# Kernel tuning notes

Hardware: AMD Instinct MI355X
Metric: run time of the kernel (lower is better)

Reference implementation:

```python
import jax, jax.numpy as jnp
import numpy as np

B, N, K, D = 4096, 64, 48, 64   # batch, n_features, n_bins, d_embedding
F = N * D                        # flattened embedding dim
E, H, O = 8, 1024, 512           # experts, expert hidden, expert out
T, TH = 2, 256                   # tasks, tower hidden


def setup_inputs() -> dict:
    key = jax.random.key(0)
    ks = jax.random.split(key, 10)
    # PLE buffers from uniform bins linspace(0,1,K+1): w = 1/width, b = -edge/width
    edges = jnp.linspace(0.0, 1.0, K + 1)
    width = jnp.diff(edges)
    w = 1.0 / width                      # (K,)
    b = -edges[:-1] / width              # (K,)
    ple_weight = jnp.broadcast_to(w, (N, K)).astype(jnp.float32)
    ple_bias = jnp.broadcast_to(b, (N, K)).astype(jnp.float32)
    s = lambda fan_in: fan_in ** -0.5
    return {
        "x": jax.random.uniform(ks[0], (B, N), jnp.float32),
        "ple_weight": ple_weight,
        "ple_bias": ple_bias,
        "emb_W": jax.random.normal(ks[1], (N, K, D), jnp.float32) * s(K),
        "emb_b": jax.random.normal(ks[2], (N, D), jnp.float32) * s(K),
        "gate_W": jax.random.normal(ks[3], (F, E), jnp.float32) * s(F),
        "gate_b": jnp.zeros((E,), jnp.float32),
        "e_W1": jax.random.normal(ks[4], (E, F, H), jnp.float32) * s(F),
        "e_b1": jnp.zeros((E, H), jnp.float32),
        "e_W2": jax.random.normal(ks[5], (E, H, O), jnp.float32) * s(H),
        "e_b2": jnp.zeros((E, O), jnp.float32),
        "tw1": jax.random.normal(ks[6], (T, O, TH), jnp.float32) * s(O),
        "tb1": jnp.zeros((T, TH), jnp.float32),
        "tw2": jax.random.normal(ks[7], (T, TH, 1), jnp.float32) * s(TH),
        "tb2": jnp.zeros((T, 1), jnp.float32),
        "top_k": 2,
    }


def reference(x, ple_weight, ple_bias, emb_W, emb_b, gate_W, gate_b,
              e_W1, e_b1, e_W2, e_b2, tw1, tb1, tw2, tb2, top_k):
    # --- Piecewise Linear Encoding: (B, N) -> (B, N, K) ---
    enc = ple_bias + ple_weight * x[..., None]
    enc = jnp.concatenate([
        jnp.minimum(enc[..., :1], 1.0),
        jnp.clip(enc[..., 1:-1], 0.0, 1.0),
        jnp.maximum(enc[..., -1:], 0.0),
    ], axis=-1)
    # --- PLE embeddings via NLinear + ReLU: (B, N, K) -> (B, N, D) ---
    emb = jax.nn.relu(jnp.einsum("bnk,nkd->bnd", enc, emb_W) + emb_b)
    flat = emb.reshape(emb.shape[0], -1)                 # (B, F)
    # --- Sparse MoE gating (softmax + top-k renormalized) ---
    probs = jax.nn.softmax(flat @ gate_W + gate_b, axis=-1)   # (B, E)
    topv, topi = jax.lax.top_k(probs, top_k)
    topv = topv / jnp.sum(topv, axis=-1, keepdims=True)
    gates = jnp.zeros_like(probs).at[jnp.arange(probs.shape[0])[:, None], topi].set(topv)
    # --- Experts (computed densely, gated combine) ---
    h = jax.nn.relu(jnp.einsum("bf,efh->beh", flat, e_W1) + e_b1)   # (B, E, H)
    eo = jnp.einsum("beh,eho->beo", h, e_W2) + e_b2                 # (B, E, O)
    moe = jnp.einsum("be,beo->bo", gates, eo)                       # (B, O)
    # --- Task towers: per-task MLP -> scalar ---
    th = jax.nn.relu(jnp.einsum("bo,tos->bts", moe, tw1) + tb1)     # (B, T, TH)
    out = (jnp.einsum("bts,tsu->btu", th, tw2) + tb2)[..., 0]       # (B, T)
    return out
```

## Files before the change

### kernel.cpp

```cpp
#include <hip/hip_runtime.h>
#include <cstdint>

#define B_ 4096
#define N_ 64
#define K_ 48
#define D_ 64
#define F_ 4096
#define E_ 8
#define H_ 1024
#define O_ 512
#define T_ 2
#define TH_ 256
#define NSLOT (B_ * 2)

#define MAXT1 72
#define MAXT2 136

typedef float f32x4 __attribute__((ext_vector_type(4)));
typedef __bf16 bf16x8 __attribute__((ext_vector_type(8)));

__device__ __forceinline__ unsigned short f2bf(float f) {
    union { float f; unsigned int u; } v; v.f = f;
    unsigned int u = v.u;
    u += 0x7FFFu + ((u >> 16) & 1u);
    return (unsigned short)(u >> 16);
}

__device__ __forceinline__ void gload_lds16(const void* gptr, void* lptr) {
    auto* g = reinterpret_cast<const __attribute__((address_space(1))) unsigned int*>(
        reinterpret_cast<uintptr_t>(gptr));
    auto* l = reinterpret_cast<__attribute__((address_space(3))) unsigned int*>(
        reinterpret_cast<uintptr_t>(lptr));
    __builtin_amdgcn_global_load_lds(g, l, 16, 0, 0);
}

__global__ __launch_bounds__(64) void prefix_kernel(
    const float* __restrict__ embW, const float* __restrict__ embB,
    float* __restrict__ P)
{
    int n = blockIdx.x;
    int lane = threadIdx.x;
    float acc = embB[n * D_ + lane];
    const float* wsrc = embW + (size_t)n * K_ * D_ + lane;
    float* dst = P + (size_t)n * K_ * D_ + lane;
    #pragma unroll 8
    for (int k = 0; k < K_; ++k) {
        dst[k * D_] = acc;
        acc += wsrc[k * D_];
    }
}

__global__ __launch_bounds__(256) void ple_embed_kernel(
    const float* __restrict__ x, const float* __restrict__ plw,
    const float* __restrict__ plb, const float* __restrict__ embW,
    const float* __restrict__ P, const float* __restrict__ gateW,
    unsigned short* __restrict__ flat_bf, float* __restrict__ logits)
{
    __shared__ float gpart[4][E_];
    int b = blockIdx.x;
    int tid = threadIdx.x, lane = tid & 63, w = tid >> 6;

    float xl = x[b * N_ + lane];
    float gp[E_];
    #pragma unroll
    for (int e = 0; e < E_; ++e) gp[e] = 0.0f;

    #pragma unroll 4
    for (int i = 0; i < 16; ++i) {
        int n = w * 16 + i;
        float xn = __shfl(xl, n);
        const float* pw = plw + n * K_;
        const float* pb = plb + n * K_;
        float t = fmaf(pw[0], xn, pb[0]);
        int j = (int)t;
        j = max(0, min(K_ - 1, j));
        float f = fminf(fmaxf(fmaf(pw[j], xn, pb[j]), 0.0f), 1.0f);
        size_t base = ((size_t)n * K_ + j) * D_ + lane;
        float emb = fmaxf(fmaf(f, embW[base], P[base]), 0.0f);
        flat_bf[(size_t)b * F_ + n * D_ + lane] = f2bf(emb);

        const float4* gw4 = (const float4*)(gateW + (size_t)(n * D_ + lane) * E_);
        float4 g0 = gw4[0], g1 = gw4[1];
        gp[0] = fmaf(emb, g0.x, gp[0]);
        gp[1] = fmaf(emb, g0.y, gp[1]);
        gp[2] = fmaf(emb, g0.z, gp[2]);
        gp[3] = fmaf(emb, g0.w, gp[3]);
        gp[4] = fmaf(emb, g1.x, gp[4]);
        gp[5] = fmaf(emb, g1.y, gp[5]);
        gp[6] = fmaf(emb, g1.z, gp[6]);
        gp[7] = fmaf(emb, g1.w, gp[7]);
    }

    #pragma unroll
    for (int off = 32; off > 0; off >>= 1) {
        #pragma unroll
        for (int e = 0; e < E_; ++e) gp[e] += __shfl_down(gp[e], off);
    }
    if (lane == 0) {
        #pragma unroll
        for (int e = 0; e < E_; ++e) gpart[w][e] = gp[e];
    }
    __syncthreads();
    if (tid < E_)
        logits[b * E_ + tid] =
            gpart[0][tid] + gpart[1][tid] + gpart[2][tid] + gpart[3][tid];
}

__global__ __launch_bounds__(256) void gate_top2_kernel(
    const float* __restrict__ logits, const float* __restrict__ gate_b,
    int* __restrict__ topi, float* __restrict__ topg, int* __restrict__ counts)
{
    int b = blockIdx.x * 256 + threadIdx.x;
    int lane = threadIdx.x & 63;
    float l[E_];
    #pragma unroll
    for (int e = 0; e < E_; ++e) l[e] = logits[b * E_ + e] + gate_b[e];
    int e1 = 0; float v1 = l[0];
    #pragma unroll
    for (int e = 1; e < E_; ++e) if (l[e] > v1) { v1 = l[e]; e1 = e; }
    int e2 = -1; float v2 = -1e30f;
    #pragma unroll
    for (int e = 0; e < E_; ++e) if (e != e1 && l[e] > v2) { v2 = l[e]; e2 = e; }
    float ex = expf(v2 - v1);
    float g1 = 1.0f / (1.0f + ex);
    float g2 = ex / (1.0f + ex);
    topi[b * 2] = e1; topi[b * 2 + 1] = e2;
    topg[b * 2] = g1; topg[b * 2 + 1] = g2;
    #pragma unroll
    for (int e = 0; e < E_; ++e) {
        unsigned long long m1 = __ballot(e1 == e);
        unsigned long long m2 = __ballot(e2 == e);
        if (lane == 0) {
            int c = __popcll(m1) + __popcll(m2);
            if (c) atomicAdd(&counts[e], c);
        }
    }
}

__global__ void scan_kernel(const int* __restrict__ counts, int* __restrict__ offsets,
                            int* __restrict__ tiles1, int* __restrict__ tiles2,
                            int* __restrict__ ntiles) {
    if (threadIdx.x == 0) {
        int s = 0, n1 = 0, n2 = 0;
        for (int e = 0; e < E_; ++e) {
            offsets[e] = s;
            int c = counts[e];
            for (int tr = 0; tr * 128 < c; ++tr) tiles1[n1++] = (e << 16) | tr;
            for (int tr = 0; tr * 64 < c; ++tr) tiles2[n2++] = (e << 16) | tr;
            s += c;
        }
        offsets[E_] = s;
        ntiles[0] = n1;
        ntiles[1] = n2;
    }
}

__global__ __launch_bounds__(256) void scatter_kernel(
    const int* __restrict__ topi, const float* __restrict__ topg,
    const int* __restrict__ offsets, int* __restrict__ cursors,
    int* __restrict__ rows, float* __restrict__ gatev)
{
    int b = blockIdx.x * 256 + threadIdx.x;
    int lane = threadIdx.x & 63;
    #pragma unroll
    for (int j = 0; j < 2; ++j) {
        int e = topi[b * 2 + j];
        float g = topg[b * 2 + j];
        #pragma unroll
        for (int ex = 0; ex < E_; ++ex) {
            unsigned long long m = __ballot(e == ex);
            if (e == ex) {
                int leader = __builtin_ctzll(m);
                int base = 0;
                if (lane == leader) base = atomicAdd(&cursors[ex], __popcll(m));
                base = __shfl(base, leader);
                int pos = base + __popcll(m & ((1ull << lane) - 1ull));
                int slot = offsets[ex] + pos;
                rows[slot] = b;
                gatev[slot] = g;
            }
        }
    }
}

__global__ __launch_bounds__(256) void transp_bf16_kernel(
    const float* __restrict__ in, unsigned short* __restrict__ out, int R, int C)
{
    __shared__ float tile[64][65];
    int ch = blockIdx.z;
    const float* src = in + (size_t)ch * R * C;
    unsigned short* dst = out + (size_t)ch * R * C;
    int c0 = blockIdx.x * 64, r0 = blockIdx.y * 64;
    int lane = threadIdx.x & 63, w = threadIdx.x >> 6;
    #pragma unroll
    for (int i = 0; i < 16; ++i) {
        int r = w * 16 + i;
        tile[r][lane] = src[(size_t)(r0 + r) * C + c0 + lane];
    }
    __syncthreads();
    #pragma unroll
    for (int i = 0; i < 16; ++i) {
        int c = w * 16 + i;
        dst[(size_t)(c0 + c) * R + r0 + lane] = f2bf(tile[lane][c]);
    }
}

__global__ __launch_bounds__(256) void fc1_kernel(
    const unsigned short* __restrict__ Abf,
    const unsigned short* __restrict__ Wbt,
    const float* __restrict__ bias,
    const int* __restrict__ rows, const int* __restrict__ offsets,
    const int* __restrict__ tiles1, const int* __restrict__ ntiles,
    unsigned short* __restrict__ Hbf)
{
    int bid = blockIdx.x;
    int tile = bid >> 4, cn = bid & 15;
    if (tile >= ntiles[0]) return;
    int te = tiles1[tile];
    int e = te >> 16, tr = te & 0xffff;
    int m0 = offsets[e], mEnd = offsets[e + 1];
    int Me = mEnd - m0;

    __shared__ alignas(16) unsigned short As[128 * 64];
    __shared__ alignas(16) unsigned short Bs[64 * 64];

    int tid = threadIdx.x, lane = tid & 63, wv = tid >> 6;
    int lr = lane >> 3;
    int pchunk = lane & 7;
    int cg = pchunk ^ lr;

    const unsigned short* aptr[4];
    const unsigned short* bptr[2];
    #pragma unroll
    for (int i = 0; i < 4; ++i) {
        int rowA = (wv * 4 + i) * 8 + lr;
        int slot = min(m0 + tr * 128 + rowA, mEnd - 1);
        aptr[i] = Abf + (size_t)rows[slot] * F_ + cg * 8;
    }
    #pragma unroll
    for (int i = 0; i < 2; ++i) {
        int rowB = cn * 64 + (wv * 2 + i) * 8 + lr;
        bptr[i] = Wbt + ((size_t)e * H_ + rowB) * (size_t)F_ + cg * 8;
    }

    f32x4 zero = {0.f, 0.f, 0.f, 0.f};
    f32x4 acc[4][2];
    #pragma unroll
    for (int i = 0; i < 4; ++i)
        #pragma unroll
        for (int j = 0; j < 2; ++j) acc[i][j] = zero;

    int wvM = wv >> 1, wvN = wv & 1;
    int m16 = lane & 15, q = lane >> 4;

    for (int k0 = 0; k0 < F_; k0 += 64) {
        __syncthreads();
        #pragma unroll
        for (int i = 0; i < 4; ++i)
            gload_lds16(aptr[i] + k0, &As[(wv * 4 + i) * 512]);
        #pragma unroll
        for (int i = 0; i < 2; ++i)
            gload_lds16(bptr[i] + k0, &Bs[(wv * 2 + i) * 512]);
        __syncthreads();
        #pragma unroll
        for (int ks = 0; ks < 2; ++ks) {
            bf16x8 af[4], bfg[2];
            #pragma unroll
            for (int mt = 0; mt < 4; ++mt) {
                int m = wvM * 64 + mt * 16 + m16;
                int pos = (ks * 4 + q) ^ (m & 7);
                af[mt] = *(const bf16x8*)&As[m * 64 + pos * 8];
            }
            #pragma unroll
            for (int nt = 0; nt < 2; ++nt) {
                int n = wvN * 32 + nt * 16 + m16;
                int pos = (ks * 4 + q) ^ (n & 7);
                bfg[nt] = *(const bf16x8*)&Bs[n * 64 + pos * 8];
            }
            #pragma unroll
            for (int mt = 0; mt < 4; ++mt)
                #pragma unroll
                for (int nt = 0; nt < 2; ++nt)
                    acc[mt][nt] = __builtin_amdgcn_mfma_f32_16x16x32_bf16(
                        af[mt], bfg[nt], acc[mt][nt], 0, 0, 0);
        }
    }

    #pragma unroll
    for (int nt = 0; nt < 2; ++nt) {
        int col = cn * 64 + wvN * 32 + nt * 16 + m16;
        float bv = bias[e * H_ + col];
        #pragma unroll
        for (int mt = 0; mt < 4; ++mt) {
            int rbase = tr * 128 + wvM * 64 + mt * 16 + q * 4;
            #pragma unroll
            for (int r = 0; r < 4; ++r) {
                int rr = rbase + r;
                if (rr < Me) {
                    float v = fmaxf(acc[mt][nt][r] + bv, 0.0f);
                    Hbf[(size_t)(m0 + rr) * H_ + col] = f2bf(v);
                }
            }
        }
    }
}

__global__ __launch_bounds__(256) void fc2_kernel(
    const unsigned short* __restrict__ Hbf,
    const unsigned short* __restrict__ Wbt,
    const float* __restrict__ bias,
    const int* __restrict__ rows, const float* __restrict__ gatev,
    const int* __restrict__ offsets, const int* __restrict__ tiles2,
    const int* __restrict__ ntiles, float* __restrict__ moe)
{
    int bid = blockIdx.x;
    int tile = bid >> 3, cn = bid & 7;
    if (tile >= ntiles[1]) return;
    int te = tiles2[tile];
    int e = te >> 16, tr = te & 0xffff;
    int m0 = offsets[e], mEnd = offsets[e + 1];
    int Me = mEnd - m0;

    __shared__ alignas(16) unsigned short As[64 * 64];
    __shared__ alignas(16) unsigned short Bs[64 * 64];

    int tid = threadIdx.x, lane = tid & 63, wv = tid >> 6;
    int lr = lane >> 3;
    int pchunk = lane & 7;
    int cg = pchunk ^ lr;

    const unsigned short* aptr[2];
    const unsigned short* bptr[2];
    #pragma unroll
    for (int i = 0; i < 2; ++i) {
        int rowA = (wv * 2 + i) * 8 + lr;
        int slot = min(m0 + tr * 64 + rowA, mEnd - 1);
        aptr[i] = Hbf + (size_t)slot * H_ + cg * 8;
        int rowB = cn * 64 + (wv * 2 + i) * 8 + lr;
        bptr[i] = Wbt + ((size_t)e * O_ + rowB) * (size_t)H_ + cg * 8;
    }

    f32x4 zero = {0.f, 0.f, 0.f, 0.f};
    f32x4 acc[4];
    #pragma unroll
    for (int i = 0; i < 4; ++i) acc[i] = zero;

    int m16 = lane & 15, q = lane >> 4;

    for (int k0 = 0; k0 < H_; k0 += 64) {
        __syncthreads();
        #pragma unroll
        for (int i = 0; i < 2; ++i) {
            gload_lds16(aptr[i] + k0, &As[(wv * 2 + i) * 512]);
            gload_lds16(bptr[i] + k0, &Bs[(wv * 2 + i) * 512]);
        }
        __syncthreads();
        #pragma unroll
        for (int ks = 0; ks < 2; ++ks) {
            bf16x8 af[4], bfg;
            #pragma unroll
            for (int mt = 0; mt < 4; ++mt) {
                int m = mt * 16 + m16;
                int pos = (ks * 4 + q) ^ (m & 7);
                af[mt] = *(const bf16x8*)&As[m * 64 + pos * 8];
            }
            {
                int n = wv * 16 + m16;
                int pos = (ks * 4 + q) ^ (n & 7);
                bfg = *(const bf16x8*)&Bs[n * 64 + pos * 8];
            }
            #pragma unroll
            for (int mt = 0; mt < 4; ++mt)
                acc[mt] = __builtin_amdgcn_mfma_f32_16x16x32_bf16(
                    af[mt], bfg, acc[mt], 0, 0, 0);
        }
    }

    int col = cn * 64 + wv * 16 + m16;
    float bv = bias[e * O_ + col];
    #pragma unroll
    for (int mt = 0; mt < 4; ++mt) {
        int rbase = tr * 64 + mt * 16 + q * 4;
        #pragma unroll
        for (int r = 0; r < 4; ++r) {
            int rr = rbase + r;
            if (rr < Me) {
                int slot = m0 + rr;
                float g = gatev[slot];
                int b = rows[slot];
                atomicAdd(&moe[(size_t)b * O_ + col], g * (acc[mt][r] + bv));
            }
        }
    }
}

__global__ __launch_bounds__(256) void tower1_kernel(
    const float* __restrict__ moe, const float* __restrict__ tw1,
    const float* __restrict__ tb1, float* __restrict__ th)
{
    __shared__ float ms[16 * O_];
    int b0 = blockIdx.x * 16;
    int tid = threadIdx.x;
    for (int idx = tid; idx < 16 * O_; idx += 256)
        ms[idx] = moe[(size_t)b0 * O_ + idx];
    __syncthreads();

    int s = tid;
    float acc0[16], acc1[16];
    float bv0 = tb1[s], bv1 = tb1[TH_ + s];
    #pragma unroll
    for (int i = 0; i < 16; ++i) { acc0[i] = bv0; acc1[i] = bv1; }

    for (int o = 0; o < O_; o += 4) {
        float w0[4], w1[4];
        #pragma unroll
        for (int u = 0; u < 4; ++u) {
            w0[u] = tw1[(size_t)(o + u) * TH_ + s];
            w1[u] = tw1[(size_t)(O_ + o + u) * TH_ + s];
        }
        #pragma unroll
        for (int smp = 0; smp < 16; ++smp) {
            float4 mv = *(const float4*)&ms[smp * O_ + o];
            acc0[smp] = fmaf(mv.x, w0[0], acc0[smp]);
            acc0[smp] = fmaf(mv.y, w0[1], acc0[smp]);
            acc0[smp] = fmaf(mv.z, w0[2], acc0[smp]);
            acc0[smp] = fmaf(mv.w, w0[3], acc0[smp]);
            acc1[smp] = fmaf(mv.x, w1[0], acc1[smp]);
            acc1[smp] = fmaf(mv.y, w1[1], acc1[smp]);
            acc1[smp] = fmaf(mv.z, w1[2], acc1[smp]);
            acc1[smp] = fmaf(mv.w, w1[3], acc1[smp]);
        }
    }
    #pragma unroll
    for (int smp = 0; smp < 16; ++smp) {
        int b = b0 + smp;
        th[((size_t)b * T_ + 0) * TH_ + s] = fmaxf(acc0[smp], 0.0f);
        th[((size_t)b * T_ + 1) * TH_ + s] = fmaxf(acc1[smp], 0.0f);
    }
}

__global__ __launch_bounds__(256) void tower2_kernel(
    const float* __restrict__ th, const float* __restrict__ tw2,
    const float* __restrict__ tb2, float* __restrict__ out)
{
    int tid = threadIdx.x, lane = tid & 63, w = tid >> 6;
    int pair = blockIdx.x * 4 + w;
    int t = pair & 1;
    const float* tp = th + (size_t)pair * TH_;
    float p = 0.0f;
    #pragma unroll
    for (int j = 0; j < TH_ / 64; ++j) {
        int s = lane + j * 64;
        p = fmaf(tp[s], tw2[t * TH_ + s], p);
    }
    #pragma unroll
    for (int off = 32; off > 0; off >>= 1) p += __shfl_down(p, off);
    if (lane == 0) out[pair] = p + tb2[t];
}

extern "C" void kernel_launch(void* const* d_in, const int* in_sizes, int n_in,
                              void* d_out, int out_size, void* d_ws, size_t ws_size,
                              hipStream_t stream)
{
    const float* x     = (const float*)d_in[0];
    const float* plw   = (const float*)d_in[1];
    const float* plb   = (const float*)d_in[2];
    const float* embW  = (const float*)d_in[3];
    const float* embB  = (const float*)d_in[4];
    const float* gateW = (const float*)d_in[5];
    const float* gateB = (const float*)d_in[6];
    const float* eW1   = (const float*)d_in[7];
    const float* eB1   = (const float*)d_in[8];
    const float* eW2   = (const float*)d_in[9];
    const float* eB2   = (const float*)d_in[10];
    const float* tw1   = (const float*)d_in[11];
    const float* tb1   = (const float*)d_in[12];
    const float* tw2   = (const float*)d_in[13];
    const float* tb2   = (const float*)d_in[14];
    float* out = (float*)d_out;

    char* w = (char*)d_ws;
    auto alloc = [&](size_t bytes) {
        char* p = w; w += (bytes + 255) & ~(size_t)255; return p;
    };
    unsigned short* flat_bf = (unsigned short*)alloc((size_t)B_ * F_ * 2);
    unsigned short* W1bt    = (unsigned short*)alloc((size_t)E_ * H_ * F_ * 2);
    unsigned short* W2bt    = (unsigned short*)alloc((size_t)E_ * O_ * H_ * 2);
    unsigned short* Hbf     = (unsigned short*)alloc((size_t)NSLOT * H_ * 2);
    float* Ppre    = (float*)alloc((size_t)N_ * K_ * D_ * 4);
    float* logits  = (float*)alloc((size_t)B_ * E_ * 4);
    float* moe     = (float*)alloc((size_t)B_ * O_ * 4);
    float* th      = (float*)alloc((size_t)B_ * T_ * TH_ * 4);
    int*   topi    = (int*)alloc((size_t)B_ * 2 * 4);
    float* topg    = (float*)alloc((size_t)B_ * 2 * 4);
    int*   rows    = (int*)alloc((size_t)NSLOT * 4);
    float* gatev   = (float*)alloc((size_t)NSLOT * 4);
    int*   counts  = (int*)alloc(E_ * 4);
    int*   offsets = (int*)alloc((E_ + 1) * 4);
    int*   cursors = (int*)alloc(E_ * 4);
    int*   tiles1  = (int*)alloc(MAXT1 * 4);
    int*   tiles2  = (int*)alloc(MAXT2 * 4);
    int*   ntiles  = (int*)alloc(2 * 4);

    hipMemsetAsync(moe, 0, (size_t)B_ * O_ * 4, stream);
    hipMemsetAsync(counts, 0, E_ * 4, stream);
    hipMemsetAsync(cursors, 0, E_ * 4, stream);

    prefix_kernel<<<N_, 64, 0, stream>>>(embW, embB, Ppre);
    ple_embed_kernel<<<B_, 256, 0, stream>>>(x, plw, plb, embW, Ppre, gateW,
                                             flat_bf, logits);
    transp_bf16_kernel<<<dim3(H_ / 64, F_ / 64, E_), 256, 0, stream>>>(eW1, W1bt, F_, H_);
    transp_bf16_kernel<<<dim3(O_ / 64, H_ / 64, E_), 256, 0, stream>>>(eW2, W2bt, H_, O_);
    gate_top2_kernel<<<B_ / 256, 256, 0, stream>>>(logits, gateB, topi, topg, counts);
    scan_kernel<<<1, 64, 0, stream>>>(counts, offsets, tiles1, tiles2, ntiles);
    scatter_kernel<<<B_ / 256, 256, 0, stream>>>(topi, topg, offsets, cursors, rows, gatev);
    fc1_kernel<<<MAXT1 * 16, 256, 0, stream>>>(flat_bf, W1bt, eB1, rows, offsets,
                                               tiles1, ntiles, Hbf);
    fc2_kernel<<<MAXT2 * 8, 256, 0, stream>>>(Hbf, W2bt, eB2, rows, gatev, offsets,
                                              tiles2, ntiles, moe);
    tower1_kernel<<<B_ / 16, 256, 0, stream>>>(moe, tw1, tb1, th);
    tower2_kernel<<<B_ * T_ / 4, 256, 0, stream>>>(th, tw2, tb2, out);
}
```

Baseline: 601.1 us.

## Enlarge expert GEMM tiles, parallelize scan, and fuse tower kernels

The fc1 tile grows from 128x64 to 128x128 output per block, with 4x4 MFMA accumulators per wave, so each weight tile is reused across more rows and fewer blocks are launched. fc2 now uses 128-row tiles that share the fc1 tile list, which removes the second tile list. The scan kernel computes offsets and tile entries with one thread per expert instead of a serial loop. The two tower kernels become one kernel that reduces the second layer in-block, removing the th intermediate buffer. In exchange, fc1 uses more registers and shared memory and launches fewer blocks, and the fused tower kernel runs at 8 rows per block.

```diff
diff --git a/kernel.cpp b/kernel.cpp
--- a/kernel.cpp
+++ b/kernel.cpp
@@ -14,7 +14,6 @@
 #define NSLOT (B_ * 2)
 
 #define MAXT1 72
-#define MAXT2 136
 
 typedef float f32x4 __attribute__((ext_vector_type(4)));
 typedef __bf16 bf16x8 __attribute__((ext_vector_type(8)));
@@ -138,21 +137,23 @@
 }
 
 __global__ void scan_kernel(const int* __restrict__ counts, int* __restrict__ offsets,
-                            int* __restrict__ tiles1, int* __restrict__ tiles2,
-                            int* __restrict__ ntiles) {
-    if (threadIdx.x == 0) {
-        int s = 0, n1 = 0, n2 = 0;
-        for (int e = 0; e < E_; ++e) {
-            offsets[e] = s;
-            int c = counts[e];
-            for (int tr = 0; tr * 128 < c; ++tr) tiles1[n1++] = (e << 16) | tr;
-            for (int tr = 0; tr * 64 < c; ++tr) tiles2[n2++] = (e << 16) | tr;
-            s += c;
-        }
-        offsets[E_] = s;
-        ntiles[0] = n1;
-        ntiles[1] = n2;
-    }
+                            int* __restrict__ tiles1, int* __restrict__ ntiles) {
+    int e = threadIdx.x;
+    if (e >= E_) return;
+    int c[E_];
+    #pragma unroll
+    for (int i = 0; i < E_; ++i) c[i] = counts[i];
+    int off = 0, tb = 0, tot = 0, ttot = 0;
+    #pragma unroll
+    for (int i = 0; i < E_; ++i) {
+        int t = (c[i] + 127) >> 7;
+        if (i < e) { off += c[i]; tb += t; }
+        tot += c[i]; ttot += t;
+    }
+    offsets[e] = off;
+    if (e == 0) { offsets[E_] = tot; ntiles[0] = ttot; }
+    int nt = (c[e] + 127) >> 7;
+    for (int tr = 0; tr < nt; ++tr) tiles1[tb + tr] = (e << 16) | tr;
 }
 
 __global__ __launch_bounds__(256) void scatter_kernel(
@@ -214,7 +215,7 @@
     unsigned short* __restrict__ Hbf)
 {
     int bid = blockIdx.x;
-    int tile = bid >> 4, cn = bid & 15;
+    int tile = bid >> 3, cn = bid & 7;
     if (tile >= ntiles[0]) return;
     int te = tiles1[tile];
     int e = te >> 16, tr = te & 0xffff;
@@ -222,7 +223,7 @@
     int Me = mEnd - m0;
 
     __shared__ alignas(16) unsigned short As[128 * 64];
-    __shared__ alignas(16) unsigned short Bs[64 * 64];
+    __shared__ alignas(16) unsigned short Bs[128 * 64];
 
     int tid = threadIdx.x, lane = tid & 63, wv = tid >> 6;
     int lr = lane >> 3;
@@ -230,25 +231,23 @@
     int cg = pchunk ^ lr;
 
     const unsigned short* aptr[4];
-    const unsigned short* bptr[2];
+    const unsigned short* bptr[4];
     #pragma unroll
     for (int i = 0; i < 4; ++i) {
-        int rowA = (wv * 4 + i) * 8 + lr;
+        int reg = wv * 4 + i;
+        int rowA = reg * 8 + lr;
         int slot = min(m0 + tr * 128 + rowA, mEnd - 1);
         aptr[i] = Abf + (size_t)rows[slot] * F_ + cg * 8;
-    }
-    #pragma unroll
-    for (int i = 0; i < 2; ++i) {
-        int rowB = cn * 64 + (wv * 2 + i) * 8 + lr;
+        int rowB = cn * 128 + reg * 8 + lr;
         bptr[i] = Wbt + ((size_t)e * H_ + rowB) * (size_t)F_ + cg * 8;
     }
 
     f32x4 zero = {0.f, 0.f, 0.f, 0.f};
-    f32x4 acc[4][2];
+    f32x4 acc[4][4];
     #pragma unroll
     for (int i = 0; i < 4; ++i)
         #pragma unroll
-        for (int j = 0; j < 2; ++j) acc[i][j] = zero;
+        for (int j = 0; j < 4; ++j) acc[i][j] = zero;
 
     int wvM = wv >> 1, wvN = wv & 1;
     int m16 = lane & 15, q = lane >> 4;
@@ -256,15 +255,15 @@
     for (int k0 = 0; k0 < F_; k0 += 64) {
         __syncthreads();
         #pragma unroll
-        for (int i = 0; i < 4; ++i)
-            gload_lds16(aptr[i] + k0, &As[(wv * 4 + i) * 512]);
-        #pragma unroll
-        for (int i = 0; i < 2; ++i)
-            gload_lds16(bptr[i] + k0, &Bs[(wv * 2 + i) * 512]);
+        for (int i = 0; i < 4; ++i) {
+            int reg = wv * 4 + i;
+            gload_lds16(aptr[i] + k0, &As[reg * 512]);
+            gload_lds16(bptr[i] + k0, &Bs[reg * 512]);
+        }
         __syncthreads();
         #pragma unroll
         for (int ks = 0; ks < 2; ++ks) {
-            bf16x8 af[4], bfg[2];
+            bf16x8 af[4], bfg[4];
             #pragma unroll
             for (int mt = 0; mt < 4; ++mt) {
                 int m = wvM * 64 + mt * 16 + m16;
@@ -272,23 +271,23 @@
                 af[mt] = *(const bf16x8*)&As[m * 64 + pos * 8];
             }
             #pragma unroll
-            for (int nt = 0; nt < 2; ++nt) {
-                int n = wvN * 32 + nt * 16 + m16;
+            for (int nt = 0; nt < 4; ++nt) {
+                int n = wvN * 64 + nt * 16 + m16;
                 int pos = (ks * 4 + q) ^ (n & 7);
                 bfg[nt] = *(const bf16x8*)&Bs[n * 64 + pos * 8];
             }
             #pragma unroll
             for (int mt = 0; mt < 4; ++mt)
                 #pragma unroll
-                for (int nt = 0; nt < 2; ++nt)
+                for (int nt = 0; nt < 4; ++nt)
                     acc[mt][nt] = __builtin_amdgcn_mfma_f32_16x16x32_bf16(
                         af[mt], bfg[nt], acc[mt][nt], 0, 0, 0);
         }
     }
 
     #pragma unroll
-    for (int nt = 0; nt < 2; ++nt) {
-        int col = cn * 64 + wvN * 32 + nt * 16 + m16;
+    for (int nt = 0; nt < 4; ++nt) {
+        int col = cn * 128 + wvN * 64 + nt * 16 + m16;
         float bv = bias[e * H_ + col];
         #pragma unroll
         for (int mt = 0; mt < 4; ++mt) {
@@ -310,18 +309,18 @@
     const unsigned short* __restrict__ Wbt,
     const float* __restrict__ bias,
     const int* __restrict__ rows, const float* __restrict__ gatev,
-    const int* __restrict__ offsets, const int* __restrict__ tiles2,
+    const int* __restrict__ offsets, const int* __restrict__ tiles1,
     const int* __restrict__ ntiles, float* __restrict__ moe)
 {
     int bid = blockIdx.x;
     int tile = bid >> 3, cn = bid & 7;
-    if (tile >= ntiles[1]) return;
-    int te = tiles2[tile];
+    if (tile >= ntiles[0]) return;
+    int te = tiles1[tile];
     int e = te >> 16, tr = te & 0xffff;
     int m0 = offsets[e], mEnd = offsets[e + 1];
     int Me = mEnd - m0;
 
-    __shared__ alignas(16) unsigned short As[64 * 64];
+    __shared__ alignas(16) unsigned short As[128 * 64];
     __shared__ alignas(16) unsigned short Bs[64 * 64];
 
     int tid = threadIdx.x, lane = tid & 63, wv = tid >> 6;
@@ -329,87 +328,102 @@
     int pchunk = lane & 7;
     int cg = pchunk ^ lr;
 
-    const unsigned short* aptr[2];
+    const unsigned short* aptr[4];
     const unsigned short* bptr[2];
     #pragma unroll
+    for (int i = 0; i < 4; ++i) {
+        int rowA = (wv * 4 + i) * 8 + lr;
+        int slot = min(m0 + tr * 128 + rowA, mEnd - 1);
+        aptr[i] = Hbf + (size_t)slot * H_ + cg * 8;
+    }
+    #pragma unroll
     for (int i = 0; i < 2; ++i) {
-        int rowA = (wv * 2 + i) * 8 + lr;
-        int slot = min(m0 + tr * 64 + rowA, mEnd - 1);
-        aptr[i] = Hbf + (size_t)slot * H_ + cg * 8;
         int rowB = cn * 64 + (wv * 2 + i) * 8 + lr;
         bptr[i] = Wbt + ((size_t)e * O_ + rowB) * (size_t)H_ + cg * 8;
     }
 
     f32x4 zero = {0.f, 0.f, 0.f, 0.f};
-    f32x4 acc[4];
-    #pragma unroll
-    for (int i = 0; i < 4; ++i) acc[i] = zero;
-
+    f32x4 acc[4][2];
+    #pragma unroll
+    for (int i = 0; i < 4; ++i)
+        #pragma unroll
+        for (int j = 0; j < 2; ++j) acc[i][j] = zero;
+
+    int wvM = wv >> 1, wvN = wv & 1;
     int m16 = lane & 15, q = lane >> 4;
 
     for (int k0 = 0; k0 < H_; k0 += 64) {
         __syncthreads();
         #pragma unroll
-        for (int i = 0; i < 2; ++i) {
-            gload_lds16(aptr[i] + k0, &As[(wv * 2 + i) * 512]);
+        for (int i = 0; i < 4; ++i)
+            gload_lds16(aptr[i] + k0, &As[(wv * 4 + i) * 512]);
+        #pragma unroll
+        for (int i = 0; i < 2; ++i)
             gload_lds16(bptr[i] + k0, &Bs[(wv * 2 + i) * 512]);
-        }
         __syncthreads();
         #pragma unroll
         for (int ks = 0; ks < 2; ++ks) {
-            bf16x8 af[4], bfg;
+            bf16x8 af[4], bfg[2];
             #pragma unroll
             for (int mt = 0; mt < 4; ++mt) {
-                int m = mt * 16 + m16;
+                int m = wvM * 64 + mt * 16 + m16;
                 int pos = (ks * 4 + q) ^ (m & 7);
                 af[mt] = *(const bf16x8*)&As[m * 64 + pos * 8];
             }
-            {
-                int n = wv * 16 + m16;
+            #pragma unroll
+            for (int nt = 0; nt < 2; ++nt) {
+                int n = wvN * 32 + nt * 16 + m16;
                 int pos = (ks * 4 + q) ^ (n & 7);
-                bfg = *(const bf16x8*)&Bs[n * 64 + pos * 8];
+                bfg[nt] = *(const bf16x8*)&Bs[n * 64 + pos * 8];
             }
             #pragma unroll
             for (int mt = 0; mt < 4; ++mt)
-                acc[mt] = __builtin_amdgcn_mfma_f32_16x16x32_bf16(
-                    af[mt], bfg, acc[mt], 0, 0, 0);
-        }
-    }
-
-    int col = cn * 64 + wv * 16 + m16;
-    float bv = bias[e * O_ + col];
-    #pragma unroll
-    for (int mt = 0; mt < 4; ++mt) {
-        int rbase = tr * 64 + mt * 16 + q * 4;
-        #pragma unroll
-        for (int r = 0; r < 4; ++r) {
-            int rr = rbase + r;
-            if (rr < Me) {
-                int slot = m0 + rr;
-                float g = gatev[slot];
-                int b = rows[slot];
-                atomicAdd(&moe[(size_t)b * O_ + col], g * (acc[mt][r] + bv));
-            }
-        }
-    }
-}
-
-__global__ __launch_bounds__(256) void tower1_kernel(
+                #pragma unroll
+                for (int nt = 0; nt < 2; ++nt)
+                    acc[mt][nt] = __builtin_amdgcn_mfma_f32_16x16x32_bf16(
+                        af[mt], bfg[nt], acc[mt][nt], 0, 0, 0);
+        }
+    }
+
+    #pragma unroll
+    for (int nt = 0; nt < 2; ++nt) {
+        int col = cn * 64 + wvN * 32 + nt * 16 + m16;
+        float bv = bias[e * O_ + col];
+        #pragma unroll
+        for (int mt = 0; mt < 4; ++mt) {
+            int rbase = tr * 128 + wvM * 64 + mt * 16 + q * 4;
+            #pragma unroll
+            for (int r = 0; r < 4; ++r) {
+                int rr = rbase + r;
+                if (rr < Me) {
+                    int slot = m0 + rr;
+                    float g = gatev[slot];
+                    int b = rows[slot];
+                    atomicAdd(&moe[(size_t)b * O_ + col], g * (acc[mt][nt][r] + bv));
+                }
+            }
+        }
+    }
+}
+
+__global__ __launch_bounds__(256) void tower_kernel(
     const float* __restrict__ moe, const float* __restrict__ tw1,
-    const float* __restrict__ tb1, float* __restrict__ th)
-{
-    __shared__ float ms[16 * O_];
-    int b0 = blockIdx.x * 16;
-    int tid = threadIdx.x;
-    for (int idx = tid; idx < 16 * O_; idx += 256)
+    const float* __restrict__ tb1, const float* __restrict__ tw2,
+    const float* __restrict__ tb2, float* __restrict__ out)
+{
+    __shared__ float ms[8 * O_];
+    __shared__ float red[16][4];
+    int b0 = blockIdx.x * 8;
+    int tid = threadIdx.x, lane = tid & 63, wv = tid >> 6;
+    for (int idx = tid; idx < 8 * O_; idx += 256)
         ms[idx] = moe[(size_t)b0 * O_ + idx];
     __syncthreads();
 
     int s = tid;
-    float acc0[16], acc1[16];
+    float a0[8], a1[8];
     float bv0 = tb1[s], bv1 = tb1[TH_ + s];
     #pragma unroll
-    for (int i = 0; i < 16; ++i) { acc0[i] = bv0; acc1[i] = bv1; }
+    for (int i = 0; i < 8; ++i) { a0[i] = bv0; a1[i] = bv1; }
 
     for (int o = 0; o < O_; o += 4) {
         float w0[4], w1[4];
@@ -419,43 +433,37 @@
             w1[u] = tw1[(size_t)(O_ + o + u) * TH_ + s];
         }
         #pragma unroll
-        for (int smp = 0; smp < 16; ++smp) {
-            float4 mv = *(const float4*)&ms[smp * O_ + o];
-            acc0[smp] = fmaf(mv.x, w0[0], acc0[smp]);
-            acc0[smp] = fmaf(mv.y, w0[1], acc0[smp]);
-            acc0[smp] = fmaf(mv.z, w0[2], acc0[smp]);
-            acc0[smp] = fmaf(mv.w, w0[3], acc0[smp]);
-            acc1[smp] = fmaf(mv.x, w1[0], acc1[smp]);
-            acc1[smp] = fmaf(mv.y, w1[1], acc1[smp]);
-            acc1[smp] = fmaf(mv.z, w1[2], acc1[smp]);
-            acc1[smp] = fmaf(mv.w, w1[3], acc1[smp]);
-        }
-    }
-    #pragma unroll
-    for (int smp = 0; smp < 16; ++smp) {
-        int b = b0 + smp;
-        th[((size_t)b * T_ + 0) * TH_ + s] = fmaxf(acc0[smp], 0.0f);
-        th[((size_t)b * T_ + 1) * TH_ + s] = fmaxf(acc1[smp], 0.0f);
-    }
-}
-
-__global__ __launch_bounds__(256) void tower2_kernel(
-    const float* __restrict__ th, const float* __restrict__ tw2,
-    const float* __restrict__ tb2, float* __restrict__ out)
-{
-    int tid = threadIdx.x, lane = tid & 63, w = tid >> 6;
-    int pair = blockIdx.x * 4 + w;
-    int t = pair & 1;
-    const float* tp = th + (size_t)pair * TH_;
-    float p = 0.0f;
-    #pragma unroll
-    for (int j = 0; j < TH_ / 64; ++j) {
-        int s = lane + j * 64;
-        p = fmaf(tp[s], tw2[t * TH_ + s], p);
-    }
-    #pragma unroll
-    for (int off = 32; off > 0; off >>= 1) p += __shfl_down(p, off);
-    if (lane == 0) out[pair] = p + tb2[t];
+        for (int i = 0; i < 8; ++i) {
+            float4 mv = *(const float4*)&ms[i * O_ + o];
+            a0[i] = fmaf(mv.x, w0[0], a0[i]);
+            a0[i] = fmaf(mv.y, w0[1], a0[i]);
+            a0[i] = fmaf(mv.z, w0[2], a0[i]);
+            a0[i] = fmaf(mv.w, w0[3], a0[i]);
+            a1[i] = fmaf(mv.x, w1[0], a1[i]);
+            a1[i] = fmaf(mv.y, w1[1], a1[i]);
+            a1[i] = fmaf(mv.z, w1[2], a1[i]);
+            a1[i] = fmaf(mv.w, w1[3], a1[i]);
+        }
+    }
+
+    float w2a = tw2[s], w2b = tw2[TH_ + s];
+    #pragma unroll
+    for (int i = 0; i < 8; ++i) {
+        float p0 = fmaxf(a0[i], 0.0f) * w2a;
+        float p1 = fmaxf(a1[i], 0.0f) * w2b;
+        #pragma unroll
+        for (int off = 32; off > 0; off >>= 1) {
+            p0 += __shfl_down(p0, off);
+            p1 += __shfl_down(p1, off);
+        }
+        if (lane == 0) { red[i * 2 + 0][wv] = p0; red[i * 2 + 1][wv] = p1; }
+    }
+    __syncthreads();
+    if (tid < 16) {
+        int i = tid >> 1, t = tid & 1;
+        float v = red[tid][0] + red[tid][1] + red[tid][2] + red[tid][3] + tb2[t];
+        out[(size_t)(b0 + i) * T_ + t] = v;
+    }
 }
 
 extern "C" void kernel_launch(void* const* d_in, const int* in_sizes, int n_in,
@@ -490,7 +498,6 @@
     float* Ppre    = (float*)alloc((size_t)N_ * K_ * D_ * 4);
     float* logits  = (float*)alloc((size_t)B_ * E_ * 4);
     float* moe     = (float*)alloc((size_t)B_ * O_ * 4);
-    float* th      = (float*)alloc((size_t)B_ * T_ * TH_ * 4);
     int*   topi    = (int*)alloc((size_t)B_ * 2 * 4);
     float* topg    = (float*)alloc((size_t)B_ * 2 * 4);
     int*   rows    = (int*)alloc((size_t)NSLOT * 4);
@@ -499,7 +506,6 @@
     int*   offsets = (int*)alloc((E_ + 1) * 4);
     int*   cursors = (int*)alloc(E_ * 4);
     int*   tiles1  = (int*)alloc(MAXT1 * 4);
-    int*   tiles2  = (int*)alloc(MAXT2 * 4);
     int*   ntiles  = (int*)alloc(2 * 4);
 
     hipMemsetAsync(moe, 0, (size_t)B_ * O_ * 4, stream);
@@ -512,12 +518,11 @@
     transp_bf16_kernel<<<dim3(H_ / 64, F_ / 64, E_), 256, 0, stream>>>(eW1, W1bt, F_, H_);
     transp_bf16_kernel<<<dim3(O_ / 64, H_ / 64, E_), 256, 0, stream>>>(eW2, W2bt, H_, O_);
     gate_top2_kernel<<<B_ / 256, 256, 0, stream>>>(logits, gateB, topi, topg, counts);
-    scan_kernel<<<1, 64, 0, stream>>>(counts, offsets, tiles1, tiles2, ntiles);
+    scan_kernel<<<1, 64, 0, stream>>>(counts, offsets, tiles1, ntiles);
     scatter_kernel<<<B_ / 256, 256, 0, stream>>>(topi, topg, offsets, cursors, rows, gatev);
-    fc1_kernel<<<MAXT1 * 16, 256, 0, stream>>>(flat_bf, W1bt, eB1, rows, offsets,
-                                               tiles1, ntiles, Hbf);
-    fc2_kernel<<<MAXT2 * 8, 256, 0, stream>>>(Hbf, W2bt, eB2, rows, gatev, offsets,
-                                              tiles2, ntiles, moe);
-    tower1_kernel<<<B_ / 16, 256, 0, stream>>>(moe, tw1, tb1, th);
-    tower2_kernel<<<B_ * T_ / 4, 256, 0, stream>>>(th, tw2, tb2, out);
-}
+    fc1_kernel<<<MAXT1 * 8, 256, 0, stream>>>(flat_bf, W1bt, eB1, rows, offsets,
+                                              tiles1, ntiles, Hbf);
+    fc2_kernel<<<MAXT1 * 8, 256, 0, stream>>>(Hbf, W2bt, eB2, rows, gatev, offsets,
+                                              tiles1, ntiles, moe);
+    tower_kernel<<<B_ / 8, 256, 0, stream>>>(moe, tw1, tb1, tw2, tb2, out);
+}
```

Result: faster. 574.8 us (-4.4%).
